# Performance work log

Measured on AMD Instinct MI355X. Metric: run time of the kernel, lower is better.

## Reference

```python
import jax, jax.numpy as jnp
import numpy as np

# Fixed-point fake quantization: 8 total bits, 4 fractional bits (STE for grads)
FRAC_BITS = 4
TOTAL_BITS = 8
SCALE = 2.0 ** FRAC_BITS
QMIN = float(-(2 ** (TOTAL_BITS - 1)))
QMAX = float(2 ** (TOTAL_BITS - 1) - 1)


def fake_quant(x):
    q = jnp.clip(jnp.round(x * SCALE), QMIN, QMAX) / SCALE
    # straight-through estimator
    return x + jax.lax.stop_gradient(q - x)


def setup_inputs() -> dict:
    key = jax.random.key(0)
    ks = jax.random.split(key, 5)
    S, B, I, H = 2048, 64, 128, 256
    std = 1.0 / np.sqrt(H)  # pytorch LSTMCell default init range
    return {
        "x": jax.random.normal(ks[0], (S, B, I), jnp.float32),
        "weight_ih": jax.random.uniform(ks[1], (4 * H, I), jnp.float32, -std, std),
        "weight_hh": jax.random.uniform(ks[2], (4 * H, H), jnp.float32, -std, std),
        "bias_ih": jax.random.uniform(ks[3], (4 * H,), jnp.float32, -std, std),
        "bias_hh": jax.random.uniform(ks[4], (4 * H,), jnp.float32, -std, std),
    }


def reference(x, weight_ih, weight_hh, bias_ih, bias_hh):
    # x: [S, B, I] (batch_first=False). Gate order i, f, g, o (pytorch LSTMCell).
    B = x.shape[1]
    H = weight_hh.shape[1]
    # weight quantization is state-independent -> hoist out of the scan
    wi = fake_quant(weight_ih)  # [4H, I]
    wh = fake_quant(weight_hh)  # [4H, H]
    bi = fake_quant(bias_ih)
    bh = fake_quant(bias_hh)

    def step(carry, x_t):
        h, c = carry
        hq = fake_quant(h)
        cq = fake_quant(c)
        gates = x_t @ wi.T + bi + hq @ wh.T + bh  # [B, 4H]
        i_g, f_g, g_g, o_g = jnp.split(gates, 4, axis=1)
        i = jax.nn.sigmoid(i_g)
        f = jax.nn.sigmoid(f_g)
        g = jnp.tanh(g_g)
        o = jax.nn.sigmoid(o_g)
        c1 = f * cq + i * g
        h1 = o * jnp.tanh(c1)
        return (h1, c1), h1

    zeros = jnp.zeros((B, H), x.dtype)
    (h_n, c_n), outputs = jax.lax.scan(step, (zeros, zeros), x)
    return outputs, h_n, c_n
```

## Files before the change

### kernel.cpp

```cpp
#include <hip/hip_runtime.h>
#include <math.h>

#define S_LEN 2048
#define BATCH 64
#define IN_D  128
#define HID   256
#define G4    1024

#if defined(__has_builtin)
# if __has_builtin(__builtin_amdgcn_sdot4)
#  define USE_SDOT4 1
# endif
#endif

__device__ __forceinline__ int dot4i8(int a, int b, int c) {
#ifdef USE_SDOT4
    return __builtin_amdgcn_sdot4(a, b, c, false);
#else
    int r = c;
    r += ((a << 24) >> 24) * ((b << 24) >> 24);
    r += ((a << 16) >> 24) * ((b << 16) >> 24);
    r += ((a <<  8) >> 24) * ((b <<  8) >> 24);
    r += ( a        >> 24) * ( b        >> 24);
    return r;
#endif
}

__device__ __forceinline__ float fq4(float x) {
    return fminf(fmaxf(rintf(x * 16.0f), -128.0f), 127.0f) * 0.0625f;
}

__device__ __forceinline__ float exp_vsl(float x) {
    const float xc = fminf(fmaxf(x, -88.3762626647949f), 88.3762626647950f);
    const float fx = floorf(fmaf(xc, 1.44269504088896341f, 0.5f));
    float r = fmaf(-fx, 0.693359375f, xc);
    r = fmaf(fx, 2.12194440e-4f, r);
    const float z = __fmul_rn(r, r);
    float y = fmaf(r, 1.9875691500e-4f, 1.3981999507e-3f);
    y = fmaf(y, r, 8.3334519073e-3f);
    y = fmaf(y, r, 4.1665795894e-2f);
    y = fmaf(y, r, 1.6666665459e-1f);
    y = fmaf(y, r, 5.0000001201e-1f);
    y = fmaf(y, z, r);
    y = __fadd_rn(y, 1.0f);
    const int n = (int)fx;
    const float sc = __int_as_float((n + 127) << 23);
    return __fmul_rn(y, sc);
}

__device__ __forceinline__ float tanh_vsl(float x) {
    const float xc = fminf(fmaxf(x, -9.0f), 9.0f);
    const float x2 = __fmul_rn(xc, xc);
    float p = -2.76076847742355e-16f;
    p = fmaf(p, x2, 2.00018790482477e-13f);
    p = fmaf(p, x2, -8.60467152213735e-11f);
    p = fmaf(p, x2, 5.12229709037114e-08f);
    p = fmaf(p, x2, 1.48572235717979e-05f);
    p = fmaf(p, x2, 6.37261928875436e-04f);
    p = fmaf(p, x2, 4.89352455891786e-03f);
    p = __fmul_rn(p, xc);
    float q = 1.19825839466702e-06f;
    q = fmaf(q, x2, 1.18534705686654e-04f);
    q = fmaf(q, x2, 2.26843463243900e-03f);
    q = fmaf(q, x2, 4.89352518554385e-03f);
    return __fdiv_rn(p, q);
}

__device__ __forceinline__ float sig_vsl(float x) {
    const float ef = exp_vsl(-x);
    return __fdiv_rn(1.0f, __fadd_rn(1.0f, ef));
}

__global__ void qlstm_prep(const float* __restrict__ wih, const float* __restrict__ whh,
                           const float* __restrict__ bih, const float* __restrict__ bhh,
                           float* __restrict__ wiq, int* __restrict__ whqT,
                           float* __restrict__ biq, float* __restrict__ bhq,
                           float* __restrict__ c_state, int* __restrict__ hq_state) {
    const int idx = blockIdx.x * 256 + threadIdx.x;
    if (idx < G4 * IN_D) wiq[idx] = fq4(wih[idx]);
    if (idx < (HID / 4) * G4) {
        const int d = idx >> 10;
        const int j = idx & 1023;
        int pack = 0;
#pragma unroll
        for (int c = 0; c < 4; ++c) {
            const int k = d * 4 + c;
            float q = fminf(fmaxf(rintf(whh[j * HID + k] * 16.0f), -128.0f), 127.0f);
            int qi = (int)q;
            pack |= (qi & 0xff) << (8 * c);
        }
        whqT[idx] = pack;
    }
    if (idx < G4) { biq[idx] = fq4(bih[idx]); bhq[idx] = fq4(bhh[idx]); }
    if (idx < BATCH * HID) c_state[idx] = 0.0f;
    if (idx < BATCH * (HID / 4)) hq_state[idx] = 0;
}

#define GPAD 132
__global__ __launch_bounds__(256, 1) void qlstm_gx(
    const float* __restrict__ X, const float* __restrict__ Wq,
    const float* __restrict__ biq, float* __restrict__ Gx, int Mc) {
    __shared__ float Xs[IN_D][GPAD];
    __shared__ float Ws[IN_D][GPAD];
    const int t  = threadIdx.x;
    const int m0 = blockIdx.x * 128;
    const int n0 = blockIdx.y * 128;

#pragma unroll
    for (int i = 0; i < 16; ++i) {
        const int flat = i * 256 + t;
        const int m  = flat >> 5;
        const int k4 = flat & 31;
        float4 v = make_float4(0.f, 0.f, 0.f, 0.f);
        if (m0 + m < Mc) v = *(const float4*)(X + (size_t)(m0 + m) * IN_D + k4 * 4);
        Xs[k4 * 4 + 0][m] = v.x; Xs[k4 * 4 + 1][m] = v.y;
        Xs[k4 * 4 + 2][m] = v.z; Xs[k4 * 4 + 3][m] = v.w;
        float4 w = *(const float4*)(Wq + (size_t)(n0 + m) * IN_D + k4 * 4);
        Ws[k4 * 4 + 0][m] = w.x; Ws[k4 * 4 + 1][m] = w.y;
        Ws[k4 * 4 + 2][m] = w.z; Ws[k4 * 4 + 3][m] = w.w;
    }
    __syncthreads();

    const int tx = t & 15, ty = t >> 4;
    float acc[8][8];
#pragma unroll
    for (int i = 0; i < 8; ++i)
#pragma unroll
        for (int j = 0; j < 8; ++j) acc[i][j] = 0.0f;

#pragma unroll 4
    for (int k = 0; k < IN_D; ++k) {
        float4 a0 = *(const float4*)&Xs[k][ty * 8];
        float4 a1 = *(const float4*)&Xs[k][ty * 8 + 4];
        float4 b0 = *(const float4*)&Ws[k][tx * 8];
        float4 b1 = *(const float4*)&Ws[k][tx * 8 + 4];
        const float a[8]  = {a0.x, a0.y, a0.z, a0.w, a1.x, a1.y, a1.z, a1.w};
        const float bb[8] = {b0.x, b0.y, b0.z, b0.w, b1.x, b1.y, b1.z, b1.w};
#pragma unroll
        for (int i = 0; i < 8; ++i)
#pragma unroll
            for (int j = 0; j < 8; ++j)
                acc[i][j] = __fadd_rn(acc[i][j], __fmul_rn(a[i], bb[j]));
    }

    float4 bv0 = *(const float4*)(biq + n0 + tx * 8);
    float4 bv1 = *(const float4*)(biq + n0 + tx * 8 + 4);
    const float bb[8] = {bv0.x, bv0.y, bv0.z, bv0.w, bv1.x, bv1.y, bv1.z, bv1.w};
#pragma unroll
    for (int i = 0; i < 8; ++i) {
        const int m = m0 + ty * 8 + i;
        if (m < Mc) {
            float o[8];
#pragma unroll
            for (int j = 0; j < 8; ++j) o[j] = __fadd_rn(acc[i][j], bb[j]);
            *(float4*)(Gx + (size_t)m * G4 + n0 + tx * 8)     = make_float4(o[0], o[1], o[2], o[3]);
            *(float4*)(Gx + (size_t)m * G4 + n0 + tx * 8 + 4) = make_float4(o[4], o[5], o[6], o[7]);
        }
    }
}

__global__ __launch_bounds__(512, 2) void qlstm_scan(
    const float* __restrict__ Gx, const int* __restrict__ whqT,
    const float* __restrict__ bhq,
    float* __restrict__ out, float* __restrict__ c_state, int* __restrict__ hq_state,
    float* __restrict__ hn, float* __restrict__ cn, int s0, int CHc) {
    const int b = blockIdx.x;
    const int t = threadIdx.x;

    __shared__ __align__(16) int hq[2][64];
    __shared__ float gl[G4];
    __shared__ float gv_s[HID], ov_s[HID];

    int w0[64], w1[64];
#pragma unroll
    for (int d = 0; d < 64; ++d) {
        w0[d] = whqT[d * G4 + t];
        w1[d] = whqT[d * G4 + t + 512];
    }
    const float bh0 = bhq[t];
    const float bh1 = bhq[t + 512];

    float creg = 0.0f;
    if (t < HID) creg = c_state[b * HID + t];
    if (t < 64)  hq[0][t] = hq_state[b * 64 + t];
    __syncthreads();

    float gx0 = Gx[(size_t)b * G4 + t];
    float gx1 = Gx[(size_t)b * G4 + t + 512];

    for (int sl = 0; sl < CHc; ++sl) {
        const int p = sl & 1;
        float nx0 = 0.0f, nx1 = 0.0f;
        if (sl + 1 < CHc) {
            const size_t base = (size_t)((sl + 1) * BATCH + b) * G4;
            nx0 = Gx[base + t];
            nx1 = Gx[base + t + 512];
        }

        int acc0 = 0, acc1 = 0;
#pragma unroll
        for (int dd = 0; dd < 16; ++dd) {
            const int4 hv = ((const int4*)hq[p])[dd];
            acc0 = dot4i8(w0[dd * 4 + 0], hv.x, acc0);
            acc0 = dot4i8(w0[dd * 4 + 1], hv.y, acc0);
            acc0 = dot4i8(w0[dd * 4 + 2], hv.z, acc0);
            acc0 = dot4i8(w0[dd * 4 + 3], hv.w, acc0);
            acc1 = dot4i8(w1[dd * 4 + 0], hv.x, acc1);
            acc1 = dot4i8(w1[dd * 4 + 1], hv.y, acc1);
            acc1 = dot4i8(w1[dd * 4 + 2], hv.z, acc1);
            acc1 = dot4i8(w1[dd * 4 + 3], hv.w, acc1);
        }
        const float hh0 = (float)acc0 * 0.00390625f;
        const float hh1 = (float)acc1 * 0.00390625f;
        gl[t]       = __fadd_rn(__fadd_rn(gx0, hh0), bh0);
        gl[t + 512] = __fadd_rn(__fadd_rn(gx1, hh1), bh1);
        __syncthreads();

        float iv = 0.0f, fv = 0.0f;
        if (t < HID) {
            iv = sig_vsl(gl[t]);
            fv = sig_vsl(gl[t + HID]);
        } else {
            const int j = t - HID;
            gv_s[j] = tanh_vsl(gl[j + 2 * HID]);
            ov_s[j] = sig_vsl(gl[j + 3 * HID]);
        }
        __syncthreads();

        if (t < HID) {
            const float cq = fminf(fmaxf(rintf(__fmul_rn(creg, 16.0f)), -128.0f), 127.0f) * 0.0625f;
            const float c1 = fmaf(fv, cq, __fmul_rn(iv, gv_s[t]));
            const float h1 = __fmul_rn(ov_s[t], tanh_vsl(c1));
            creg = c1;
            out[(size_t)((s0 + sl) * BATCH + b) * HID + t] = h1;
            const int hb = (int)fminf(fmaxf(rintf(__fmul_rn(h1, 16.0f)), -128.0f), 127.0f);
            ((signed char*)hq[p ^ 1])[t] = (signed char)hb;
            if (s0 + sl == S_LEN - 1) {
                hn[b * HID + t] = h1;
                cn[b * HID + t] = c1;
            }
        }
        __syncthreads();
        gx0 = nx0; gx1 = nx1;
    }

    if (t < 64)  hq_state[b * 64 + t] = hq[CHc & 1][t];
    if (t < HID) c_state[b * HID + t] = creg;
}

extern "C" void kernel_launch(void* const* d_in, const int* in_sizes, int n_in,
                              void* d_out, int out_size, void* d_ws, size_t ws_size,
                              hipStream_t stream) {
    (void)in_sizes; (void)n_in; (void)out_size;
    const float* x   = (const float*)d_in[0];
    const float* wih = (const float*)d_in[1];
    const float* whh = (const float*)d_in[2];
    const float* bih = (const float*)d_in[3];
    const float* bhh = (const float*)d_in[4];

    float* out = (float*)d_out;
    float* hn  = out + (size_t)S_LEN * BATCH * HID;
    float* cn  = hn + (size_t)BATCH * HID;

    char* ws = (char*)d_ws;
    const size_t off_wiq  = 0;
    const size_t off_whqT = off_wiq  + 524288;
    const size_t off_biq  = off_whqT + 262144;
    const size_t off_bhq  = off_biq  + 4096;
    const size_t off_c    = off_bhq  + 4096;
    const size_t off_hq   = off_c    + 65536;
    const size_t off_gx   = off_hq   + 16384;

    float* wiq     = (float*)(ws + off_wiq);
    int*   whqT    = (int*)  (ws + off_whqT);
    float* biq     = (float*)(ws + off_biq);
    float* bhq     = (float*)(ws + off_bhq);
    float* c_state = (float*)(ws + off_c);
    int*   hq_st   = (int*)  (ws + off_hq);
    float* gx      = (float*)(ws + off_gx);

    const size_t per_step = (size_t)BATCH * G4 * 4;
    size_t avail = (ws_size > off_gx) ? (ws_size - off_gx) : 0;
    int CH = (int)(avail / per_step);
    if (CH > S_LEN) CH = S_LEN;
    if (CH < 1) CH = 1;

    qlstm_prep<<<512, 256, 0, stream>>>(wih, whh, bih, bhh, wiq, whqT, biq, bhq, c_state, hq_st);

    for (int s0 = 0; s0 < S_LEN; s0 += CH) {
        const int CHc = (S_LEN - s0 < CH) ? (S_LEN - s0) : CH;
        const int Mc  = CHc * BATCH;
        dim3 grid((Mc + 127) / 128, G4 / 128);
        qlstm_gx<<<grid, 256, 0, stream>>>(x + (size_t)s0 * BATCH * IN_D, wiq, biq, gx, Mc);
        qlstm_scan<<<64, 512, 0, stream>>>(gx, whqT, bhq, out, c_state, hq_st, hn, cn, s0, CHc);
    }
}
```

Baseline: 3.066 ms.

## Compute gate activations in registers and remove one barrier per step

Each thread now applies its nonlinearity directly to the gate values it computes instead of staging all 1024 gates in shared memory. Thread t holds gates t and t+512, so threads below 256 take i and g and the rest take f and o. Only f and o go through shared memory, as a float2, which removes one __syncthreads and a shared-memory round trip from every serial timestep. The int8 dot-product accumulation is also split into four independent chains to shorten the dependency latency. The remaining work is the per-step latency-bound recurrence, and the change keeps its arithmetic order the same except for the integer partial sums.

```diff
diff --git a/kernel.cpp b/kernel.cpp
--- a/kernel.cpp
+++ b/kernel.cpp
@@ -168,8 +168,7 @@
     const int t = threadIdx.x;
 
     __shared__ __align__(16) int hq[2][64];
-    __shared__ float gl[G4];
-    __shared__ float gv_s[HID], ov_s[HID];
+    __shared__ float2 fo_s[HID];
 
     int w0[64], w1[64];
 #pragma unroll
@@ -197,40 +196,48 @@
             nx1 = Gx[base + t + 512];
         }
 
-        int acc0 = 0, acc1 = 0;
-#pragma unroll
-        for (int dd = 0; dd < 16; ++dd) {
-            const int4 hv = ((const int4*)hq[p])[dd];
-            acc0 = dot4i8(w0[dd * 4 + 0], hv.x, acc0);
-            acc0 = dot4i8(w0[dd * 4 + 1], hv.y, acc0);
-            acc0 = dot4i8(w0[dd * 4 + 2], hv.z, acc0);
-            acc0 = dot4i8(w0[dd * 4 + 3], hv.w, acc0);
-            acc1 = dot4i8(w1[dd * 4 + 0], hv.x, acc1);
-            acc1 = dot4i8(w1[dd * 4 + 1], hv.y, acc1);
-            acc1 = dot4i8(w1[dd * 4 + 2], hv.z, acc1);
-            acc1 = dot4i8(w1[dd * 4 + 3], hv.w, acc1);
-        }
+        int c0a[4] = {0, 0, 0, 0};
+        int c1a[4] = {0, 0, 0, 0};
+#pragma unroll
+        for (int j = 0; j < 4; ++j) {
+#pragma unroll
+            for (int d = 0; d < 4; ++d) {
+                const int4 hv = ((const int4*)hq[p])[j * 4 + d];
+                const int base = (j * 4 + d) * 4;
+                c0a[j] = dot4i8(w0[base + 0], hv.x, c0a[j]);
+                c0a[j] = dot4i8(w0[base + 1], hv.y, c0a[j]);
+                c0a[j] = dot4i8(w0[base + 2], hv.z, c0a[j]);
+                c0a[j] = dot4i8(w0[base + 3], hv.w, c0a[j]);
+                c1a[j] = dot4i8(w1[base + 0], hv.x, c1a[j]);
+                c1a[j] = dot4i8(w1[base + 1], hv.y, c1a[j]);
+                c1a[j] = dot4i8(w1[base + 2], hv.z, c1a[j]);
+                c1a[j] = dot4i8(w1[base + 3], hv.w, c1a[j]);
+            }
+        }
+        const int acc0 = (c0a[0] + c0a[1]) + (c0a[2] + c0a[3]);
+        const int acc1 = (c1a[0] + c1a[1]) + (c1a[2] + c1a[3]);
+
         const float hh0 = (float)acc0 * 0.00390625f;
         const float hh1 = (float)acc1 * 0.00390625f;
-        gl[t]       = __fadd_rn(__fadd_rn(gx0, hh0), bh0);
-        gl[t + 512] = __fadd_rn(__fadd_rn(gx1, hh1), bh1);
+        const float gate0 = __fadd_rn(__fadd_rn(gx0, hh0), bh0);
+        const float gate1 = __fadd_rn(__fadd_rn(gx1, hh1), bh1);
+
+        float iv = 0.0f, gv = 0.0f;
+        if (t < HID) {
+            iv = sig_vsl(gate0);
+            gv = tanh_vsl(gate1);
+        } else {
+            const float fv = sig_vsl(gate0);
+            const float ov = sig_vsl(gate1);
+            fo_s[t - HID] = make_float2(fv, ov);
+        }
         __syncthreads();
 
-        float iv = 0.0f, fv = 0.0f;
         if (t < HID) {
-            iv = sig_vsl(gl[t]);
-            fv = sig_vsl(gl[t + HID]);
-        } else {
-            const int j = t - HID;
-            gv_s[j] = tanh_vsl(gl[j + 2 * HID]);
-            ov_s[j] = sig_vsl(gl[j + 3 * HID]);
-        }
-        __syncthreads();
-
-        if (t < HID) {
+            const float2 fo = fo_s[t];
             const float cq = fminf(fmaxf(rintf(__fmul_rn(creg, 16.0f)), -128.0f), 127.0f) * 0.0625f;
-            const float c1 = fmaf(fv, cq, __fmul_rn(iv, gv_s[t]));
-            const float h1 = __fmul_rn(ov_s[t], tanh_vsl(c1));
+            const float c1 = fmaf(fo.x, cq, __fmul_rn(iv, gv));
+            const float h1 = __fmul_rn(fo.y, tanh_vsl(c1));
             creg = c1;
             out[(size_t)((s0 + sl) * BATCH + b) * HID + t] = h1;
             const int hb = (int)fminf(fmaxf(rintf(__fmul_rn(h1, 16.0f)), -128.0f), 127.0f);
```

Result: faster. 2.980 ms (-2.8%).

## Use one thread per gate column in LSTM scan and drop a barrier

Applied to the files above, without the earlier changes.

The recurrent scan kernel now launches 1024 threads per batch block instead of 512, so each thread owns a single gate column and holds 64 weight registers instead of 128. Each thread applies its gate's activation right after the dot product, which removes one of the three barriers per timestep and the separate activation phase. The dot product is split into four independent accumulators to shorten the dependency chain. The cost is more wavefronts per block contending at the remaining barriers, and register pressure under the 1024-thread launch bound.

```diff
diff --git a/kernel.cpp b/kernel.cpp
--- a/kernel.cpp
+++ b/kernel.cpp
@@ -159,7 +159,7 @@
     }
 }
 
-__global__ __launch_bounds__(512, 2) void qlstm_scan(
+__global__ __launch_bounds__(1024, 4) void qlstm_scan(
     const float* __restrict__ Gx, const int* __restrict__ whqT,
     const float* __restrict__ bhq,
     float* __restrict__ out, float* __restrict__ c_state, int* __restrict__ hq_state,
@@ -169,68 +169,68 @@
 
     __shared__ __align__(16) int hq[2][64];
     __shared__ float gl[G4];
-    __shared__ float gv_s[HID], ov_s[HID];
-
-    int w0[64], w1[64];
-#pragma unroll
-    for (int d = 0; d < 64; ++d) {
-        w0[d] = whqT[d * G4 + t];
-        w1[d] = whqT[d * G4 + t + 512];
-    }
-    const float bh0 = bhq[t];
-    const float bh1 = bhq[t + 512];
+
+    int w[64];
+#pragma unroll
+    for (int d = 0; d < 64; ++d) w[d] = whqT[d * G4 + t];
+
+    const float bh = bhq[t];
 
     float creg = 0.0f;
     if (t < HID) creg = c_state[b * HID + t];
     if (t < 64)  hq[0][t] = hq_state[b * 64 + t];
     __syncthreads();
 
-    float gx0 = Gx[(size_t)b * G4 + t];
-    float gx1 = Gx[(size_t)b * G4 + t + 512];
+    float gx = Gx[(size_t)b * G4 + t];
 
     for (int sl = 0; sl < CHc; ++sl) {
         const int p = sl & 1;
-        float nx0 = 0.0f, nx1 = 0.0f;
-        if (sl + 1 < CHc) {
-            const size_t base = (size_t)((sl + 1) * BATCH + b) * G4;
-            nx0 = Gx[base + t];
-            nx1 = Gx[base + t + 512];
-        }
-
-        int acc0 = 0, acc1 = 0;
-#pragma unroll
-        for (int dd = 0; dd < 16; ++dd) {
-            const int4 hv = ((const int4*)hq[p])[dd];
-            acc0 = dot4i8(w0[dd * 4 + 0], hv.x, acc0);
-            acc0 = dot4i8(w0[dd * 4 + 1], hv.y, acc0);
-            acc0 = dot4i8(w0[dd * 4 + 2], hv.z, acc0);
-            acc0 = dot4i8(w0[dd * 4 + 3], hv.w, acc0);
-            acc1 = dot4i8(w1[dd * 4 + 0], hv.x, acc1);
-            acc1 = dot4i8(w1[dd * 4 + 1], hv.y, acc1);
-            acc1 = dot4i8(w1[dd * 4 + 2], hv.z, acc1);
-            acc1 = dot4i8(w1[dd * 4 + 3], hv.w, acc1);
-        }
-        const float hh0 = (float)acc0 * 0.00390625f;
-        const float hh1 = (float)acc1 * 0.00390625f;
-        gl[t]       = __fadd_rn(__fadd_rn(gx0, hh0), bh0);
-        gl[t + 512] = __fadd_rn(__fadd_rn(gx1, hh1), bh1);
+        float nx = 0.0f;
+        if (sl + 1 < CHc) nx = Gx[(size_t)((sl + 1) * BATCH + b) * G4 + t];
+
+        int ca0 = 0, ca1 = 0, ca2 = 0, ca3 = 0;
+#pragma unroll
+        for (int d = 0; d < 4; ++d) {
+            const int4 h0 = ((const int4*)hq[p])[d];
+            const int4 h1 = ((const int4*)hq[p])[4 + d];
+            const int4 h2 = ((const int4*)hq[p])[8 + d];
+            const int4 h3 = ((const int4*)hq[p])[12 + d];
+            ca0 = dot4i8(w[d * 4 + 0], h0.x, ca0);
+            ca0 = dot4i8(w[d * 4 + 1], h0.y, ca0);
+            ca0 = dot4i8(w[d * 4 + 2], h0.z, ca0);
+            ca0 = dot4i8(w[d * 4 + 3], h0.w, ca0);
+            ca1 = dot4i8(w[16 + d * 4 + 0], h1.x, ca1);
+            ca1 = dot4i8(w[16 + d * 4 + 1], h1.y, ca1);
+            ca1 = dot4i8(w[16 + d * 4 + 2], h1.z, ca1);
+            ca1 = dot4i8(w[16 + d * 4 + 3], h1.w, ca1);
+            ca2 = dot4i8(w[32 + d * 4 + 0], h2.x, ca2);
+            ca2 = dot4i8(w[32 + d * 4 + 1], h2.y, ca2);
+            ca2 = dot4i8(w[32 + d * 4 + 2], h2.z, ca2);
+            ca2 = dot4i8(w[32 + d * 4 + 3], h2.w, ca2);
+            ca3 = dot4i8(w[48 + d * 4 + 0], h3.x, ca3);
+            ca3 = dot4i8(w[48 + d * 4 + 1], h3.y, ca3);
+            ca3 = dot4i8(w[48 + d * 4 + 2], h3.z, ca3);
+            ca3 = dot4i8(w[48 + d * 4 + 3], h3.w, ca3);
+        }
+        const int acc = (ca0 + ca1) + (ca2 + ca3);
+
+        const float hh = (float)acc * 0.00390625f;
+        const float gate = __fadd_rn(__fadd_rn(gx, hh), bh);
+
+        float tv;
+        if (t < 512)       tv = sig_vsl(gate);
+        else if (t < 768)  tv = tanh_vsl(gate);
+        else               tv = sig_vsl(gate);
+        gl[t] = tv;
         __syncthreads();
 
-        float iv = 0.0f, fv = 0.0f;
         if (t < HID) {
-            iv = sig_vsl(gl[t]);
-            fv = sig_vsl(gl[t + HID]);
-        } else {
-            const int j = t - HID;
-            gv_s[j] = tanh_vsl(gl[j + 2 * HID]);
-            ov_s[j] = sig_vsl(gl[j + 3 * HID]);
-        }
-        __syncthreads();
-
-        if (t < HID) {
+            const float fv = gl[t + 256];
+            const float gv = gl[t + 512];
+            const float ov = gl[t + 768];
             const float cq = fminf(fmaxf(rintf(__fmul_rn(creg, 16.0f)), -128.0f), 127.0f) * 0.0625f;
-            const float c1 = fmaf(fv, cq, __fmul_rn(iv, gv_s[t]));
-            const float h1 = __fmul_rn(ov_s[t], tanh_vsl(c1));
+            const float c1 = fmaf(fv, cq, __fmul_rn(tv, gv));
+            const float h1 = __fmul_rn(ov, tanh_vsl(c1));
             creg = c1;
             out[(size_t)((s0 + sl) * BATCH + b) * HID + t] = h1;
             const int hb = (int)fminf(fmaxf(rintf(__fmul_rn(h1, 16.0f)), -128.0f), 127.0f);
@@ -241,7 +241,7 @@
             }
         }
         __syncthreads();
-        gx0 = nx0; gx1 = nx1;
+        gx = nx;
     }
 
     if (t < 64)  hq_state[b * 64 + t] = hq[CHc & 1][t];
@@ -292,6 +292,6 @@
         const int Mc  = CHc * BATCH;
         dim3 grid((Mc + 127) / 128, G4 / 128);
         qlstm_gx<<<grid, 256, 0, stream>>>(x + (size_t)s0 * BATCH * IN_D, wiq, biq, gx, Mc);
-        qlstm_scan<<<64, 512, 0, stream>>>(gx, whqT, bhq, out, c_state, hq_st, hn, cn, s0, CHc);
-    }
-}
+        qlstm_scan<<<64, 1024, 0, stream>>>(gx, whqT, bhq, out, c_state, hq_st, hn, cn, s0, CHc);
+    }
+}
```

After: 3.111 ms. Within noise of the previous version (+1.5%).
